# Optimization experiments

Measured on AMD Instinct MI355X. Metric: run time of the kernel, lower is better.

The kernel has to match this reference:

```python
import jax, jax.numpy as jnp
import numpy as np

N_ENTITIES = 100000
N_RELATIONS = 100
EMB = 64         # entity embedding_size
REL_DIM = 64     # relation_dim
BATCH = 65536


def setup_inputs() -> dict:
    key = jax.random.key(0)
    k1, k2, k3, k4, k5, k6 = jax.random.split(key, 6)
    head = jax.random.randint(k1, (BATCH,), 0, N_ENTITIES)
    relation = jax.random.randint(k2, (BATCH,), 0, N_RELATIONS)
    tail = jax.random.randint(k3, (BATCH,), 0, N_ENTITIES)
    entity_emb = jax.random.normal(k4, (N_ENTITIES, EMB), dtype=jnp.float32)
    relation_emb = jax.random.normal(k5, (N_RELATIONS, REL_DIM), dtype=jnp.float32)
    proj_emb = jax.random.normal(k6, (N_RELATIONS, EMB * REL_DIM), dtype=jnp.float32)
    return {
        "head": head,
        "relation": relation,
        "tail": tail,
        "entity_emb": entity_emb,
        "relation_emb": relation_emb,
        "proj_emb": proj_emb,
    }


def reference(head, relation, tail, entity_emb, relation_emb, proj_emb):
    h_emb = entity_emb[head]                           # [B, E]
    t_emb = entity_emb[tail]                           # [B, E]
    r_emb = relation_emb[relation]                     # [B, R]
    proj = proj_emb[relation].reshape(-1, EMB, REL_DIM)  # [B, E, R]
    h_proj = jnp.einsum('be,ber->br', h_emb, proj)     # [B, R]
    t_proj = jnp.einsum('be,ber->br', t_emb, proj)     # [B, R]
    diff = h_proj + r_emb - t_proj
    score = jnp.sum(diff * diff, axis=1)               # [B]
    return score
```

## Files before the change

### kernel.cpp

```cpp
#include <hip/hip_runtime.h>

#define BATCH   65536
#define NREL    100
#define NBB     64
#define NTILE   16

typedef __attribute__((ext_vector_type(8))) short bf16x8;
typedef __attribute__((ext_vector_type(4))) float f32x4;

__device__ __forceinline__ unsigned short f2bf(float x) {
    unsigned u = __float_as_uint(x);
    u += 0x7fffu + ((u >> 16) & 1u);
    return (unsigned short)(u >> 16);
}

__launch_bounds__(256)
__global__ void transr_prep(const int* __restrict__ relation,
                            const float* __restrict__ proj,
                            int* __restrict__ ws_hist,
                            int* __restrict__ ws_lpfx,
                            int* __restrict__ ws_bucket,
                            unsigned short* __restrict__ ws_pbf) {
    const int tid = threadIdx.x, bid = blockIdx.x;

    if (bid < NBB) {
        __shared__ int hist[NREL];
        __shared__ int scan[128];

        for (int r = tid; r < NREL; r += 256) hist[r] = 0;
        __syncthreads();

        const int4 v = ((const int4*)relation)[bid * 256 + tid];
        const int vals[4] = {v.x, v.y, v.z, v.w};
        int lr[4];
        #pragma unroll
        for (int k = 0; k < 4; ++k) lr[k] = atomicAdd(&hist[vals[k]], 1);
        __syncthreads();

        if (tid < 128) scan[tid] = (tid < NREL) ? hist[tid] : 0;
        __syncthreads();
        #pragma unroll
        for (int off = 1; off < 128; off <<= 1) {
            int t = 0;
            if (tid < 128 && tid >= off) t = scan[tid - off];
            __syncthreads();
            if (tid < 128) scan[tid] += t;
            __syncthreads();
        }

        const int i0 = (bid * 256 + tid) * 4;
        #pragma unroll
        for (int k = 0; k < 4; ++k) {
            const int rel = vals[k];
            ws_bucket[bid * 1024 + (scan[rel] - hist[rel]) + lr[k]] = i0 + k;
        }
        for (int r = tid; r < NREL; r += 256) {
            ws_hist[r * NBB + bid] = hist[r];
            ws_lpfx[r * NBB + bid] = scan[r] - hist[r];
        }
    } else {
        const int rel = bid - NBB;
        const int n = tid >> 2, q = tid & 3;
        const float* Pr = proj + (size_t)rel * 4096;
        unsigned short* dst = ws_pbf + (size_t)rel * 4096;
        #pragma unroll
        for (int kh = 0; kh < 2; ++kh) {
            const int khi = q * 2 + kh;
            unsigned short u[8];
            #pragma unroll
            for (int klo = 0; klo < 8; ++klo)
                u[klo] = f2bf(Pr[(khi * 8 + klo) * 64 + n]);
            *(bf16x8*)&dst[n * 64 + ((khi ^ (n & 7)) << 3)] = *(bf16x8*)u;
        }
    }
}

__launch_bounds__(256)
__global__ void transr_compute(const int* __restrict__ head,
                               const int* __restrict__ tail,
                               const float* __restrict__ ent,
                               const float* __restrict__ remb,
                               const int* __restrict__ ws_hist,
                               const int* __restrict__ ws_lpfx,
                               const int* __restrict__ ws_bucket,
                               const unsigned short* __restrict__ ws_pbf,
                               float* __restrict__ out) {
    __shared__ unsigned short Abuf[64 * 64];
    __shared__ unsigned short Bbuf[64 * 64];
    __shared__ float remb_s[64];
    __shared__ int   pfx_s[64];
    __shared__ int   lpfx_s[64];
    __shared__ int   bidx_s[64];
    __shared__ int   cnt_s;

    const int tid   = threadIdx.x;
    const int wid   = tid >> 6;
    const int lane  = tid & 63;
    const int rel   = blockIdx.y;
    const int start = blockIdx.x << 6;

    if (wid == 0) {
        int h = ws_hist[rel * NBB + lane];
        lpfx_s[lane] = ws_lpfx[rel * NBB + lane];
        const int own = h;
        #pragma unroll
        for (int m = 1; m < 64; m <<= 1) {
            int t = __shfl_up(h, m);
            if (lane >= m) h += t;
        }
        pfx_s[lane] = h - own;
        if (lane == 63) cnt_s = h;
    }
    if (tid < 64) remb_s[tid] = remb[rel * 64 + tid];
    __syncthreads();

    const int cnt = cnt_s;
    if (start >= cnt) return;

    {
        const int row = tid >> 2, q = tid & 3;
        const int j  = start + row;
        const int jj = (j < cnt) ? j : (cnt - 1);
        int lo = 0;
        #pragma unroll
        for (int s = 32; s; s >>= 1) {
            const int c = lo + s;
            if (c < 64 && pfx_s[c] <= jj) lo = c;
        }
        const int b = ws_bucket[lo * 1024 + lpfx_s[lo] + (jj - pfx_s[lo])];
        if (q == 0) bidx_s[row] = b;
        const int h = head[b], t = tail[b];
        const float4* h4 = (const float4*)(ent + (size_t)h * 64) + q * 4;
        const float4* t4 = (const float4*)(ent + (size_t)t * 64) + q * 4;
        #pragma unroll
        for (int i = 0; i < 2; ++i) {
            unsigned short u[8];
            #pragma unroll
            for (int m = 0; m < 2; ++m) {
                float4 a = h4[i * 2 + m], c = t4[i * 2 + m];
                u[m * 4 + 0] = f2bf(a.x - c.x);
                u[m * 4 + 1] = f2bf(a.y - c.y);
                u[m * 4 + 2] = f2bf(a.z - c.z);
                u[m * 4 + 3] = f2bf(a.w - c.w);
            }
            const int slice = (q * 2 + i) ^ (row & 7);
            *(bf16x8*)&Abuf[row * 64 + slice * 8] = *(bf16x8*)u;
        }
    }
    {
        const uint4* src = (const uint4*)(ws_pbf + (size_t)rel * 4096) + tid * 2;
        uint4* dst = (uint4*)Bbuf + tid * 2;
        dst[0] = src[0];
        dst[1] = src[1];
    }
    __syncthreads();

    const int arow = wid * 16 + (lane & 15);
    const int g    = lane >> 4;

    f32x4 acc[4];
    #pragma unroll
    for (int f = 0; f < 4; ++f) {
        const float rv = remb_s[f * 16 + (lane & 15)];
        acc[f] = (f32x4){rv, rv, rv, rv};
    }
    #pragma unroll
    for (int s = 0; s < 2; ++s) {
        const int ks = g + s * 4;
        bf16x8 av = *(const bf16x8*)&Abuf[arow * 64 + ((ks ^ (arow & 7)) * 8)];
        #pragma unroll
        for (int f = 0; f < 4; ++f) {
            const int col = f * 16 + (lane & 15);
            bf16x8 bv = *(const bf16x8*)&Bbuf[col * 64 + ((ks ^ (col & 7)) * 8)];
            acc[f] = __builtin_amdgcn_mfma_f32_16x16x32_bf16(av, bv, acc[f], 0, 0, 0);
        }
    }

    float ps[4];
    #pragma unroll
    for (int r = 0; r < 4; ++r)
        ps[r] = acc[0][r] * acc[0][r] + acc[1][r] * acc[1][r] +
                acc[2][r] * acc[2][r] + acc[3][r] * acc[3][r];
    #pragma unroll
    for (int m = 1; m < 16; m <<= 1) {
        #pragma unroll
        for (int r = 0; r < 4; ++r) ps[r] += __shfl_xor(ps[r], m, 64);
    }
    if ((lane & 15) == 0) {
        const int rowb = wid * 16 + g * 4;
        #pragma unroll
        for (int r = 0; r < 4; ++r) {
            const int j = start + rowb + r;
            if (j < cnt) out[bidx_s[rowb + r]] = ps[r];
        }
    }
}

extern "C" void kernel_launch(void* const* d_in, const int* in_sizes, int n_in,
                              void* d_out, int out_size, void* d_ws, size_t ws_size,
                              hipStream_t stream) {
    const int*   head     = (const int*)d_in[0];
    const int*   relation = (const int*)d_in[1];
    const int*   tail     = (const int*)d_in[2];
    const float* ent      = (const float*)d_in[3];
    const float* remb     = (const float*)d_in[4];
    const float* proj     = (const float*)d_in[5];
    float*       out      = (float*)d_out;

    int* ws_hist   = (int*)d_ws;
    int* ws_lpfx   = (int*)d_ws + 8192;
    int* ws_bucket = (int*)d_ws + 16384;
    unsigned short* ws_pbf =
        (unsigned short*)((char*)d_ws + 512 * 1024);

    transr_prep<<<NBB + NREL, 256, 0, stream>>>(relation, proj,
                                                ws_hist, ws_lpfx, ws_bucket, ws_pbf);
    transr_compute<<<dim3(NTILE, NREL), 256, 0, stream>>>(
        head, tail, ent, remb, ws_hist, ws_lpfx, ws_bucket, ws_pbf, out);
}
```

Measured before the change: 21.05 us.

## Double compute tile to 128 rows and replace shared prefix scan with per-wave shuffles

The compute kernel now uses 512-thread blocks that each handle 128 sorted rows, with a grid of 8 x 100 instead of 16 x 100. Each wave recomputes the histogram prefix scan in registers and looks values up with shuffles, so the shared-memory prefix arrays and the first __syncthreads are gone. The projection image load is issued early into registers, and the relation-embedding accumulator init now reads straight from global memory. This trades fewer blocks and less per-block sync for more redundant scan work per wave and a larger shared-memory footprint per block.

```diff
diff --git a/kernel.cpp b/kernel.cpp
--- a/kernel.cpp
+++ b/kernel.cpp
@@ -3,7 +3,7 @@
 #define BATCH   65536
 #define NREL    100
 #define NBB     64
-#define NTILE   16
+#define NBX     8
 
 typedef __attribute__((ext_vector_type(8))) short bf16x8;
 typedef __attribute__((ext_vector_type(4))) float f32x4;
@@ -75,7 +75,7 @@
     }
 }
 
-__launch_bounds__(256)
+__launch_bounds__(512)
 __global__ void transr_compute(const int* __restrict__ head,
                                const int* __restrict__ tail,
                                const float* __restrict__ ent,
@@ -85,37 +85,29 @@
                                const int* __restrict__ ws_bucket,
                                const unsigned short* __restrict__ ws_pbf,
                                float* __restrict__ out) {
-    __shared__ unsigned short Abuf[64 * 64];
+    __shared__ unsigned short Abuf[128 * 64];
     __shared__ unsigned short Bbuf[64 * 64];
-    __shared__ float remb_s[64];
-    __shared__ int   pfx_s[64];
-    __shared__ int   lpfx_s[64];
-    __shared__ int   bidx_s[64];
-    __shared__ int   cnt_s;
+    __shared__ int bidx_s[128];
 
     const int tid   = threadIdx.x;
     const int wid   = tid >> 6;
     const int lane  = tid & 63;
     const int rel   = blockIdx.y;
-    const int start = blockIdx.x << 6;
-
-    if (wid == 0) {
-        int h = ws_hist[rel * NBB + lane];
-        lpfx_s[lane] = ws_lpfx[rel * NBB + lane];
-        const int own = h;
-        #pragma unroll
-        for (int m = 1; m < 64; m <<= 1) {
-            int t = __shfl_up(h, m);
-            if (lane >= m) h += t;
-        }
-        pfx_s[lane] = h - own;
-        if (lane == 63) cnt_s = h;
-    }
-    if (tid < 64) remb_s[tid] = remb[rel * 64 + tid];
-    __syncthreads();
-
-    const int cnt = cnt_s;
+    const int start = blockIdx.x << 7;
+
+    const int hown = ws_hist[rel * NBB + lane];
+    const int lpfx = ws_lpfx[rel * NBB + lane];
+    int hinc = hown;
+    #pragma unroll
+    for (int m = 1; m < 64; m <<= 1) {
+        int t = __shfl_up(hinc, m);
+        if (lane >= m) hinc += t;
+    }
+    const int hexc = hinc - hown;
+    const int cnt  = __shfl(hinc, 63);
     if (start >= cnt) return;
+
+    const uint4 bimg = ((const uint4*)(ws_pbf + (size_t)rel * 4096))[tid];
 
     {
         const int row = tid >> 2, q = tid & 3;
@@ -125,9 +117,10 @@
         #pragma unroll
         for (int s = 32; s; s >>= 1) {
             const int c = lo + s;
-            if (c < 64 && pfx_s[c] <= jj) lo = c;
-        }
-        const int b = ws_bucket[lo * 1024 + lpfx_s[lo] + (jj - pfx_s[lo])];
+            const int v = __shfl(hexc, c & 63);
+            if (c < 64 && v <= jj) lo = c;
+        }
+        const int b = ws_bucket[lo * 1024 + __shfl(lpfx, lo) + (jj - __shfl(hexc, lo))];
         if (q == 0) bidx_s[row] = b;
         const int h = head[b], t = tail[b];
         const float4* h4 = (const float4*)(ent + (size_t)h * 64) + q * 4;
@@ -147,23 +140,20 @@
             *(bf16x8*)&Abuf[row * 64 + slice * 8] = *(bf16x8*)u;
         }
     }
-    {
-        const uint4* src = (const uint4*)(ws_pbf + (size_t)rel * 4096) + tid * 2;
-        uint4* dst = (uint4*)Bbuf + tid * 2;
-        dst[0] = src[0];
-        dst[1] = src[1];
-    }
+    ((uint4*)Bbuf)[tid] = bimg;
+
+    const float* Rr = remb + rel * 64;
+    f32x4 acc[4];
+    #pragma unroll
+    for (int f = 0; f < 4; ++f) {
+        const float rv = Rr[f * 16 + (lane & 15)];
+        acc[f] = (f32x4){rv, rv, rv, rv};
+    }
+
     __syncthreads();
 
     const int arow = wid * 16 + (lane & 15);
     const int g    = lane >> 4;
-
-    f32x4 acc[4];
-    #pragma unroll
-    for (int f = 0; f < 4; ++f) {
-        const float rv = remb_s[f * 16 + (lane & 15)];
-        acc[f] = (f32x4){rv, rv, rv, rv};
-    }
     #pragma unroll
     for (int s = 0; s < 2; ++s) {
         const int ks = g + s * 4;
@@ -215,6 +205,6 @@
 
     transr_prep<<<NBB + NREL, 256, 0, stream>>>(relation, proj,
                                                 ws_hist, ws_lpfx, ws_bucket, ws_pbf);
-    transr_compute<<<dim3(NTILE, NREL), 256, 0, stream>>>(
+    transr_compute<<<dim3(NBX, NREL), 512, 0, stream>>>(
         head, tail, ent, remb, ws_hist, ws_lpfx, ws_bucket, ws_pbf, out);
 }
```

Result: slower. 22.29 us (+5.9%).
